# Kernel tuning notes

Hardware: AMD Instinct MI355X
Metric: run time of the kernel (lower is better)

Reference implementation:

```python
import jax, jax.numpy as jnp
import numpy as np
from jax import lax

B, P = 32, 1024          # batch, max_phonemes
V, E, H = 100, 512, 512  # vocab, embedding_dim, hidden_dim
EPS = 1e-5


def setup_inputs() -> dict:
    key = jax.random.key(0)
    ks = jax.random.split(key, 12)
    return {
        "phoneme_ids": jax.random.randint(ks[0], (B, P), 0, V),
        "phoneme_durations": jax.random.randint(ks[1], (B, P), 0, 10),
        "emb": jax.random.normal(ks[2], (V, E), jnp.float32) * 0.02,
        "conv1_w": jax.random.normal(ks[3], (H, E, 3), jnp.float32) * 0.02,
        "conv1_b": jnp.zeros((H,), jnp.float32),
        "bn1_gamma": 1.0 + 0.1 * jax.random.normal(ks[4], (H,), jnp.float32),
        "bn1_beta": 0.1 * jax.random.normal(ks[5], (H,), jnp.float32),
        "bn1_mean": jnp.zeros((H,), jnp.float32),
        "bn1_var": jnp.ones((H,), jnp.float32),
        "conv2_w": jax.random.normal(ks[6], (H, H, 3), jnp.float32) * 0.02,
        "conv2_b": jnp.zeros((H,), jnp.float32),
        "bn2_gamma": 1.0 + 0.1 * jax.random.normal(ks[7], (H,), jnp.float32),
        "bn2_beta": 0.1 * jax.random.normal(ks[8], (H,), jnp.float32),
        "bn2_mean": jnp.zeros((H,), jnp.float32),
        "bn2_var": jnp.ones((H,), jnp.float32),
    }


def _conv_bn_relu(x, w, b, gamma, beta, mean, var):
    # x: [B, C, P]; w: [O, C, 3]; 'same' padding conv1d, inference batchnorm, relu
    y = lax.conv_general_dilated(x, w, (1,), [(1, 1)],
                                 dimension_numbers=("NCH", "OIH", "NCH"))
    y = y + b[None, :, None]
    scale = gamma * lax.rsqrt(var + EPS)
    y = y * scale[None, :, None] + (beta - mean * scale)[None, :, None]
    return jax.nn.relu(y)


def _upsample(x, durations):
    # x: [B, H, P], durations: [B, P] int -> [B, H, max_frames]
    cum = jnp.cumsum(durations, axis=1)              # [B, P]
    total = cum[:, -1]                               # [B]
    max_frames = int(jnp.max(total))                 # concrete (data-derived shape)
    frames = jnp.arange(max_frames)                  # [F]
    # frame f belongs to phoneme p iff cum[p-1] <= f < cum[p]
    idx = jax.vmap(lambda c: jnp.searchsorted(c, frames, side="right"))(cum)
    idx = jnp.minimum(idx, P - 1)                    # [B, F]
    gathered = jnp.take_along_axis(x, idx[:, None, :], axis=2)  # [B, H, F]
    mask = (frames[None, :] < total[:, None]).astype(x.dtype)   # [B, F]
    return gathered * mask[:, None, :]


def reference(phoneme_ids, phoneme_durations, emb,
              conv1_w, conv1_b, bn1_gamma, bn1_beta, bn1_mean, bn1_var,
              conv2_w, conv2_b, bn2_gamma, bn2_beta, bn2_mean, bn2_var):
    x = emb[phoneme_ids]                 # [B, P, E]
    x = jnp.transpose(x, (0, 2, 1))      # [B, E, P]
    x = _conv_bn_relu(x, conv1_w, conv1_b, bn1_gamma, bn1_beta, bn1_mean, bn1_var)
    x = _conv_bn_relu(x, conv2_w, conv2_b, bn2_gamma, bn2_beta, bn2_mean, bn2_var)
    return _upsample(x, phoneme_durations)
```

## Files before the change

kernel.cpp:

```cpp
#include <hip/hip_runtime.h>

#define B_ 32
#define P_ 1024
#define V_ 100
#define E_ 512
#define H_ 512
#define C_ 512
#define EPS_ 1e-5f

typedef float f32x4 __attribute__((ext_vector_type(4)));
typedef short bf16x8 __attribute__((ext_vector_type(8)));

#define GLB(p) ((const __attribute__((address_space(1))) unsigned int*)(p))
#define LDSP(p) ((__attribute__((address_space(3))) unsigned int*)(p))

__device__ __forceinline__ unsigned short f2bf(float f) {
  unsigned int u = __float_as_uint(f);
  u += 0x7fffu + ((u >> 16) & 1u);
  return (unsigned short)(u >> 16);
}
__device__ __forceinline__ float bf2f(unsigned short s) {
  return __uint_as_float(((unsigned int)s) << 16);
}

__global__ __launch_bounds__(256) void w1t_kernel(const float* __restrict__ w1,
                                                  float* __restrict__ w1T) {
  __shared__ float tile[64][65];
  int h0 = blockIdx.x * 64;
  int e0 = blockIdx.y * 64;
  int t = threadIdx.x;
  int c = t & 63, r4 = t >> 6;
#pragma unroll
  for (int r = 0; r < 64; r += 4)
    tile[r + r4][c] = w1[(size_t)(h0 + r + r4) * 1536 + e0 + c];
  __syncthreads();
#pragma unroll
  for (int r = 0; r < 64; r += 4)
    w1T[(size_t)(e0 + r + r4) * 512 + h0 + c] = tile[c][r + r4];
}

__global__ __launch_bounds__(64) void g_kernel(const float* __restrict__ emb,
                                               const float* __restrict__ w1T,
                                               const float* __restrict__ g1,
                                               const float* __restrict__ vr1,
                                               float* __restrict__ G) {
  __shared__ float se[E_];
  int v = blockIdx.x;
  int h = blockIdx.y * 64 + threadIdx.x;
  for (int i = threadIdx.x; i < E_; i += 64) se[i] = emb[(size_t)v * E_ + i];
  __syncthreads();
  float a0 = 0.f, a1 = 0.f, a2 = 0.f;
#pragma unroll 4
  for (int e = 0; e < E_; ++e) {
    float x = se[e];
    const float* wp = w1T + (size_t)(3 * e) * H_ + h;
    a0 = fmaf(wp[0], x, a0);
    a1 = fmaf(wp[H_], x, a1);
    a2 = fmaf(wp[2 * H_], x, a2);
  }
  float sc = g1[h] * rsqrtf(vr1[h] + EPS_);
  G[((size_t)0 * V_ + v) * H_ + h] = a0 * sc;
  G[((size_t)1 * V_ + v) * H_ + h] = a1 * sc;
  G[((size_t)2 * V_ + v) * H_ + h] = a2 * sc;
}

__global__ __launch_bounds__(256) void a2_kernel(
    const float* __restrict__ w2, const float* __restrict__ b1,
    const float* __restrict__ g1, const float* __restrict__ be1,
    const float* __restrict__ mn1, const float* __restrict__ vr1,
    const float* __restrict__ b2, const float* __restrict__ g2,
    const float* __restrict__ be2, const float* __restrict__ mn2,
    const float* __restrict__ vr2, float* __restrict__ bias1,
    float* __restrict__ bias2, unsigned short* __restrict__ A2h,
    unsigned short* __restrict__ A2l) {
  int h = blockIdx.x;
  int tid = threadIdx.x;
  float sc1 = g1[h] * rsqrtf(vr1[h] + EPS_);
  float sc2 = g2[h] * rsqrtf(vr2[h] + EPS_);
  if (tid == 0) {
    bias1[h] = b1[h] * sc1 + be1[h] - mn1[h] * sc1;
    bias2[h] = b2[h] * sc2 + be2[h] - mn2[h] * sc2;
  }
  for (int j = tid; j < 3 * C_; j += 256) {
    int k = j >> 9;
    int c = j & (C_ - 1);
    float val = w2[((size_t)h * C_ + c) * 3 + k] * sc2;
    unsigned short hi = f2bf(val);
    A2h[(size_t)h * (3 * C_) + j] = hi;
    A2l[(size_t)h * (3 * C_) + j] = f2bf(val - bf2f(hi));
  }
}

__global__ __launch_bounds__(256) void embed_conv1_kernel(
    const int* __restrict__ ids, const float* __restrict__ G,
    const float* __restrict__ bias1, unsigned short* __restrict__ Bh,
    unsigned short* __restrict__ Bl) {
  int r = blockIdx.x % (P_ + 2);
  int b = blockIdx.x / (P_ + 2);
  int t = threadIdx.x;
  size_t outbase = ((size_t)b * (P_ + 2) + r) * C_;
  unsigned int* BhU = (unsigned int*)(Bh + outbase);
  unsigned int* BlU = (unsigned int*)(Bl + outbase);
  if (r == 0 || r == P_ + 1) {
    BhU[t] = 0u;
    BlU[t] = 0u;
    return;
  }
  int p = r - 1;
  int v0 = (p >= 1) ? ids[b * P_ + p - 1] : -1;
  int v1 = ids[b * P_ + p];
  int v2 = (p + 1 < P_) ? ids[b * P_ + p + 1] : -1;
  const float2* G0 = (v0 >= 0) ? (const float2*)(G + ((size_t)0 * V_ + v0) * H_) : nullptr;
  const float2* G1 = (const float2*)(G + ((size_t)1 * V_ + v1) * H_);
  const float2* G2 = (v2 >= 0) ? (const float2*)(G + ((size_t)2 * V_ + v2) * H_) : nullptr;
  const float2* bi = (const float2*)bias1;

  float2 s = bi[t];
  float2 gm = G1[t];
  s.x += gm.x;
  s.y += gm.y;
  if (G0) {
    float2 g0 = G0[t];
    s.x += g0.x;
    s.y += g0.y;
  }
  if (G2) {
    float2 g2v = G2[t];
    s.x += g2v.x;
    s.y += g2v.y;
  }
  s.x = fmaxf(s.x, 0.f);
  s.y = fmaxf(s.y, 0.f);
  unsigned short h0 = f2bf(s.x), h1 = f2bf(s.y);
  unsigned short l0 = f2bf(s.x - bf2f(h0)), l1 = f2bf(s.y - bf2f(h1));
  BhU[t] = (unsigned int)h0 | ((unsigned int)h1 << 16);
  BlU[t] = (unsigned int)l0 | ((unsigned int)l1 << 16);
}

__global__ __launch_bounds__(1024) void cumsum_kernel(const int* __restrict__ dur,
                                                      int* __restrict__ cum) {
  __shared__ int s[P_];
  int b = blockIdx.x;
  int t = threadIdx.x;
  s[t] = dur[b * P_ + t];
  __syncthreads();
  for (int off = 1; off < P_; off <<= 1) {
    int v = (t >= off) ? s[t - off] : 0;
    __syncthreads();
    s[t] += v;
    __syncthreads();
  }
  cum[b * P_ + t] = s[t];
}

#define BM 128
#define BN 128
#define BK 32
__global__ __launch_bounds__(256) void conv2_gemm_kernel(
    const unsigned short* __restrict__ A2h, const unsigned short* __restrict__ A2l,
    const unsigned short* __restrict__ Bh, const unsigned short* __restrict__ Bl,
    const float* __restrict__ bias2, float* __restrict__ out2) {
  __shared__ __align__(16) unsigned short lds[4][BM * BK];

  int tid = threadIdx.x;
  int w = tid >> 6;
  int l = tid & 63;

  int bid = blockIdx.x;
  int wg = ((bid & 7) << 7) | (bid >> 3);
  int m0 = (wg >> 8) * BM;
  int n0 = (wg & 255) * BN;
  int b = n0 >> 10;
  int p0 = n0 & (P_ - 1);

  const unsigned short* Ah_base = A2h + (size_t)m0 * (3 * C_);
  const unsigned short* Al_base = A2l + (size_t)m0 * (3 * C_);
  const unsigned short* Bh_base = Bh + ((size_t)b * (P_ + 2) + p0) * C_;
  const unsigned short* Bl_base = Bl + ((size_t)b * (P_ + 2) + p0) * C_;

  f32x4 acc[4][4] = {};

  int srow = l >> 2;
  int scol = (l & 3) * 8;
  int fr = l & 15, fq = l >> 4;
  int wr = (w >> 1) * 64, wc = (w & 1) * 64;

  for (int kt = 0; kt < (3 * C_) / BK; ++kt) {
    int kofs = kt * BK;
#pragma unroll
    for (int q = 0; q < 2; ++q) {
      int seg = q * 4 + w;
      int row = seg * 16 + srow;
      int col = kofs + scol;
      __builtin_amdgcn_global_load_lds(GLB(Ah_base + (size_t)row * (3 * C_) + col),
                                       LDSP(&lds[0][seg * 512]), 16, 0, 0);
      __builtin_amdgcn_global_load_lds(GLB(Al_base + (size_t)row * (3 * C_) + col),
                                       LDSP(&lds[1][seg * 512]), 16, 0, 0);
      __builtin_amdgcn_global_load_lds(GLB(Bh_base + (size_t)row * C_ + col),
                                       LDSP(&lds[2][seg * 512]), 16, 0, 0);
      __builtin_amdgcn_global_load_lds(GLB(Bl_base + (size_t)row * C_ + col),
                                       LDSP(&lds[3][seg * 512]), 16, 0, 0);
    }
    __syncthreads();

    bf16x8 ah[4], al[4], bh[4], bl[4];
#pragma unroll
    for (int i = 0; i < 4; ++i) {
      ah[i] = *(const bf16x8*)&lds[0][(wr + i * 16 + fr) * BK + fq * 8];
      al[i] = *(const bf16x8*)&lds[1][(wr + i * 16 + fr) * BK + fq * 8];
    }
#pragma unroll
    for (int j = 0; j < 4; ++j) {
      bh[j] = *(const bf16x8*)&lds[2][(wc + j * 16 + fr) * BK + fq * 8];
      bl[j] = *(const bf16x8*)&lds[3][(wc + j * 16 + fr) * BK + fq * 8];
    }
#pragma unroll
    for (int i = 0; i < 4; ++i)
#pragma unroll
      for (int j = 0; j < 4; ++j) {
        acc[i][j] = __builtin_amdgcn_mfma_f32_16x16x32_bf16(ah[i], bh[j], acc[i][j], 0, 0, 0);
        acc[i][j] = __builtin_amdgcn_mfma_f32_16x16x32_bf16(ah[i], bl[j], acc[i][j], 0, 0, 0);
        acc[i][j] = __builtin_amdgcn_mfma_f32_16x16x32_bf16(al[i], bh[j], acc[i][j], 0, 0, 0);
      }
    __syncthreads();
  }

#pragma unroll
  for (int i = 0; i < 4; ++i) {
#pragma unroll
    for (int j = 0; j < 4; ++j) {
#pragma unroll
      for (int r = 0; r < 4; ++r) {
        int m = m0 + wr + i * 16 + fq * 4 + r;
        int n = n0 + wc + j * 16 + fr;
        int bb = n >> 10;
        int p = n & (P_ - 1);
        float v = acc[i][j][r] + bias2[m];
        v = fmaxf(v, 0.f);
        out2[((size_t)bb * H_ + m) * P_ + p] = v;
      }
    }
  }
}

__global__ __launch_bounds__(256) void upsample_kernel(const float* __restrict__ out2,
                                                       const int* __restrict__ cum,
                                                       float* __restrict__ out, int T) {
  __shared__ int sc[P_];
  int b = blockIdx.y;
  int tid = threadIdx.x;
  for (int i = tid; i < P_; i += 256) sc[i] = cum[b * P_ + i];
  __syncthreads();
  int t = blockIdx.x * 256 + tid;
  if (t >= T) return;
  int tot = sc[P_ - 1];
  bool valid = (t < tot);
  int idx = 0;
  if (valid) {
    int lo = 0, hi = P_;
    while (lo < hi) {
      int mid = (lo + hi) >> 1;
      if (sc[mid] <= t) lo = mid + 1; else hi = mid;
    }
    idx = min(lo, P_ - 1);
  }
  const float* src = out2 + (size_t)b * H_ * P_ + idx;
  float* dst = out + (size_t)b * H_ * T + t;
  if (valid) {
    for (int h = 0; h < H_; ++h) dst[(size_t)h * T] = src[(size_t)h * P_];
  } else {
    for (int h = 0; h < H_; ++h) dst[(size_t)h * T] = 0.f;
  }
}

static inline size_t align256(size_t x) { return (x + 255) & ~(size_t)255; }

extern "C" void kernel_launch(void* const* d_in, const int* in_sizes, int n_in,
                              void* d_out, int out_size, void* d_ws, size_t ws_size,
                              hipStream_t stream) {
  const int*   ids = (const int*)d_in[0];
  const int*   dur = (const int*)d_in[1];
  const float* emb = (const float*)d_in[2];
  const float* w1  = (const float*)d_in[3];
  const float* b1  = (const float*)d_in[4];
  const float* g1  = (const float*)d_in[5];
  const float* be1 = (const float*)d_in[6];
  const float* mn1 = (const float*)d_in[7];
  const float* vr1 = (const float*)d_in[8];
  const float* w2  = (const float*)d_in[9];
  const float* b2  = (const float*)d_in[10];
  const float* g2  = (const float*)d_in[11];
  const float* be2 = (const float*)d_in[12];
  const float* mn2 = (const float*)d_in[13];
  const float* vr2 = (const float*)d_in[14];
  float* out = (float*)d_out;

  int T = out_size / (B_ * H_);

  char* ws = (char*)d_ws;
  size_t off = 0;
  auto carve = [&](size_t bytes) { void* p = ws + off; off = align256(off + bytes); return p; };
  float* G              = (float*)carve((size_t)3 * V_ * H_ * 4);
  float* w1T            = (float*)carve((size_t)3 * E_ * H_ * 4);
  float* bias1          = (float*)carve(H_ * 4);
  float* bias2          = (float*)carve(H_ * 4);
  unsigned short* A2h   = (unsigned short*)carve((size_t)H_ * 3 * C_ * 2);
  unsigned short* A2l   = (unsigned short*)carve((size_t)H_ * 3 * C_ * 2);
  unsigned short* Bhv   = (unsigned short*)carve((size_t)B_ * (P_ + 2) * C_ * 2);
  unsigned short* Blv   = (unsigned short*)carve((size_t)B_ * (P_ + 2) * C_ * 2);
  float* out2           = (float*)carve((size_t)B_ * H_ * P_ * 4);
  int* cum              = (int*)carve((size_t)B_ * P_ * 4);

  w1t_kernel<<<dim3(H_ / 64, (3 * E_) / 64), 256, 0, stream>>>(w1, w1T);
  a2_kernel<<<H_, 256, 0, stream>>>(w2, b1, g1, be1, mn1, vr1, b2, g2, be2, mn2, vr2,
                                    bias1, bias2, A2h, A2l);
  g_kernel<<<dim3(V_, H_ / 64), 64, 0, stream>>>(emb, w1T, g1, vr1, G);
  embed_conv1_kernel<<<B_ * (P_ + 2), 256, 0, stream>>>(ids, G, bias1, Bhv, Blv);
  cumsum_kernel<<<B_, P_, 0, stream>>>(dur, cum);
  conv2_gemm_kernel<<<(B_ * P_ / BN) * (H_ / BM), 256, 0, stream>>>(A2h, A2l, Bhv, Blv,
                                                                    bias2, out2);
  upsample_kernel<<<dim3((T + 255) / 256, B_), 256, 0, stream>>>(out2, cum, out, T);
}
```

Measured before the change: 698.3 us.

## Rewrite conv2 GEMM as 256x256 double-buffered 8-wave pipeline; vectorize upsample per thread

Replaces the 128x128 single-buffer conv2 GEMM with a 256x256 tile, 512-thread kernel. It double-buffers LDS with swizzled layout, interleaves global-to-LDS staging with MFMA quads, and uses explicit barriers and priority hints. The three split-bf16 products are reformulated as a concatenated K loop over hi/lo segments. The upsample kernel now handles four frames per thread to reduce block count and amortize work. The intent is to overlap memory with MFMA and improve reuse, at the cost of more complex synchronization and higher register pressure.

```diff
diff --git a/kernel.cpp b/kernel.cpp
--- a/kernel.cpp
+++ b/kernel.cpp
@@ -119,16 +119,8 @@
   float2 gm = G1[t];
   s.x += gm.x;
   s.y += gm.y;
-  if (G0) {
-    float2 g0 = G0[t];
-    s.x += g0.x;
-    s.y += g0.y;
-  }
-  if (G2) {
-    float2 g2v = G2[t];
-    s.x += g2v.x;
-    s.y += g2v.y;
-  }
+  if (G0) { float2 g0 = G0[t]; s.x += g0.x; s.y += g0.y; }
+  if (G2) { float2 g2v = G2[t]; s.x += g2v.x; s.y += g2v.y; }
   s.x = fmaxf(s.x, 0.f);
   s.y = fmaxf(s.y, 0.f);
   unsigned short h0 = f2bf(s.x), h1 = f2bf(s.y);
@@ -153,94 +145,182 @@
   cum[b * P_ + t] = s[t];
 }
 
-#define BM 128
-#define BN 128
-#define BK 32
-__global__ __launch_bounds__(256) void conv2_gemm_kernel(
+struct BTrue  { static constexpr bool v = true;  };
+struct BFalse { static constexpr bool v = false; };
+
+__global__ __launch_bounds__(512, 2) void conv2_gemm8_kernel(
     const unsigned short* __restrict__ A2h, const unsigned short* __restrict__ A2l,
     const unsigned short* __restrict__ Bh, const unsigned short* __restrict__ Bl,
     const float* __restrict__ bias2, float* __restrict__ out2) {
-  __shared__ __align__(16) unsigned short lds[4][BM * BK];
-
-  int tid = threadIdx.x;
-  int w = tid >> 6;
-  int l = tid & 63;
+  __shared__ __align__(16) unsigned short sm[4][16384];
+
+  const int tid = threadIdx.x;
+  const int wid = tid >> 6;
+  const int lane = tid & 63;
+  const int wm = wid >> 2, wn = wid & 3;
+  const int fr = lane & 15, fq = lane >> 4;
 
   int bid = blockIdx.x;
-  int wg = ((bid & 7) << 7) | (bid >> 3);
-  int m0 = (wg >> 8) * BM;
-  int n0 = (wg & 255) * BN;
-  int b = n0 >> 10;
+  int wg = (bid & 7) * 32 + (bid >> 3);
+  int m0 = (wg & 1) * 256;
+  int n0 = (wg >> 1) * 256;
+  int bb = n0 >> 10;
   int p0 = n0 & (P_ - 1);
 
-  const unsigned short* Ah_base = A2h + (size_t)m0 * (3 * C_);
-  const unsigned short* Al_base = A2l + (size_t)m0 * (3 * C_);
-  const unsigned short* Bh_base = Bh + ((size_t)b * (P_ + 2) + p0) * C_;
-  const unsigned short* Bl_base = Bl + ((size_t)b * (P_ + 2) + p0) * C_;
-
-  f32x4 acc[4][4] = {};
-
-  int srow = l >> 2;
-  int scol = (l & 3) * 8;
-  int fr = l & 15, fq = l >> 4;
-  int wr = (w >> 1) * 64, wc = (w & 1) * 64;
-
-  for (int kt = 0; kt < (3 * C_) / BK; ++kt) {
-    int kofs = kt * BK;
-#pragma unroll
-    for (int q = 0; q < 2; ++q) {
-      int seg = q * 4 + w;
-      int row = seg * 16 + srow;
-      int col = kofs + scol;
-      __builtin_amdgcn_global_load_lds(GLB(Ah_base + (size_t)row * (3 * C_) + col),
-                                       LDSP(&lds[0][seg * 512]), 16, 0, 0);
-      __builtin_amdgcn_global_load_lds(GLB(Al_base + (size_t)row * (3 * C_) + col),
-                                       LDSP(&lds[1][seg * 512]), 16, 0, 0);
-      __builtin_amdgcn_global_load_lds(GLB(Bh_base + (size_t)row * C_ + col),
-                                       LDSP(&lds[2][seg * 512]), 16, 0, 0);
-      __builtin_amdgcn_global_load_lds(GLB(Bl_base + (size_t)row * C_ + col),
-                                       LDSP(&lds[3][seg * 512]), 16, 0, 0);
+  const unsigned short* Arow_h = A2h + (size_t)m0 * 1536;
+  const unsigned short* Arow_l = A2l + (size_t)m0 * 1536;
+  const size_t boff = ((size_t)bb * (P_ + 2) + p0) * 512;
+  const unsigned short* Brow_h = Bh + boff;
+  const unsigned short* Brow_l = Bl + boff;
+
+  const int srow = tid >> 3;
+  const int scol = (((tid & 7) ^ ((tid >> 3) & 7))) * 8;
+  const int ldsw = wid * 512;
+
+  auto stageA = [&](int kt, int blk) {
+    const unsigned short* base = (kt < 48) ? Arow_h : Arow_l;
+    int kl = (kt % 24) * 64;
+    const unsigned short* src = base + (size_t)(blk * 64 + srow) * 1536 + kl + scol;
+    __builtin_amdgcn_global_load_lds(GLB(src), LDSP(&sm[kt & 1][blk * 4096 + ldsw]), 16, 0, 0);
+  };
+  auto stageB = [&](int kt, int blk) {
+    const unsigned short* base = (kt >= 24 && kt < 48) ? Brow_l : Brow_h;
+    int kl = (kt % 24) * 64;
+    const unsigned short* src = base + (size_t)(blk * 64 + srow) * 512 + kl + scol;
+    __builtin_amdgcn_global_load_lds(GLB(src), LDSP(&sm[2 + (kt & 1)][blk * 4096 + ldsw]), 16, 0, 0);
+  };
+
+  f32x4 acc[8][4] = {};
+
+  const int rA0 = wm * 128 + fr;
+  const int rB0 = wn * 64 + fr;
+  const int cxor = fr & 7;
+
+  auto rdA = [&](bf16x8 (&af)[4][2], int buf, int mh) {
+#pragma unroll
+    for (int m = 0; m < 4; ++m)
+#pragma unroll
+      for (int ks = 0; ks < 2; ++ks)
+        af[m][ks] = *(const bf16x8*)&sm[buf][(rA0 + mh * 64 + m * 16) * 64 +
+                                            ((ks * 4 + fq) ^ cxor) * 8];
+  };
+  auto rdB = [&](bf16x8 (&bv)[2][2], int buf, int nh) {
+#pragma unroll
+    for (int n = 0; n < 2; ++n)
+#pragma unroll
+      for (int ks = 0; ks < 2; ++ks)
+        bv[n][ks] = *(const bf16x8*)&sm[2 + buf][(rB0 + nh * 32 + n * 16) * 64 +
+                                                 ((ks * 4 + fq) ^ cxor) * 8];
+  };
+
+#define SYNC_HEAD()                                      \
+  __builtin_amdgcn_sched_barrier(0);                     \
+  __builtin_amdgcn_s_barrier();                          \
+  asm volatile("s_waitcnt lgkmcnt(0)" ::: "memory");     \
+  __builtin_amdgcn_sched_barrier(0);                     \
+  __builtin_amdgcn_s_setprio(1)
+
+#define SYNC_TAIL()                                      \
+  __builtin_amdgcn_s_setprio(0);                         \
+  __builtin_amdgcn_sched_barrier(0);                     \
+  __builtin_amdgcn_s_barrier();                          \
+  __builtin_amdgcn_sched_barrier(0)
+
+#define MFMA_QUAD(mh, nh, AF, BF)                                              \
+  _Pragma("unroll") for (int m = 0; m < 4; ++m)                                \
+  _Pragma("unroll") for (int n = 0; n < 2; ++n)                                \
+  _Pragma("unroll") for (int ks = 0; ks < 2; ++ks)                             \
+    acc[(mh) * 4 + m][(nh) * 2 + n] = __builtin_amdgcn_mfma_f32_16x16x32_bf16( \
+        AF[m][ks], BF[n][ks], acc[(mh) * 4 + m][(nh) * 2 + n], 0, 0, 0)
+
+#pragma unroll
+  for (int blk = 0; blk < 4; ++blk) { stageA(0, blk); stageB(0, blk); }
+  stageA(1, 0); stageA(1, 2);
+  asm volatile("s_waitcnt vmcnt(2)" ::: "memory");
+  __builtin_amdgcn_sched_barrier(0);
+  __builtin_amdgcn_s_barrier();
+  __builtin_amdgcn_sched_barrier(0);
+
+  int kt = 0;
+  auto iter = [&](auto lasttag) {
+    constexpr bool LAST = decltype(lasttag)::v;
+    bf16x8 af[4][2], bv[2][2];
+    rdA(af, 0, 0); rdB(bv, 0, 0);
+    stageA(kt + 1, 1); stageA(kt + 1, 3); stageB(kt + 1, 0);
+    SYNC_HEAD(); MFMA_QUAD(0, 0, af, bv); SYNC_TAIL();
+
+    rdB(bv, 0, 1);
+    stageB(kt + 1, 1); stageB(kt + 1, 2); stageB(kt + 1, 3);
+    SYNC_HEAD(); MFMA_QUAD(0, 1, af, bv); SYNC_TAIL();
+
+    rdA(af, 0, 1); rdB(bv, 0, 0);
+    if constexpr (!LAST) { stageA(kt + 2, 0); stageA(kt + 2, 2); }
+    SYNC_HEAD(); MFMA_QUAD(1, 0, af, bv); SYNC_TAIL();
+
+    rdB(bv, 0, 1);
+    __builtin_amdgcn_sched_barrier(0);
+    __builtin_amdgcn_s_barrier();
+    asm volatile("s_waitcnt lgkmcnt(0)" ::: "memory");
+    __builtin_amdgcn_sched_barrier(0);
+    __builtin_amdgcn_s_setprio(1);
+    MFMA_QUAD(1, 1, af, bv);
+    __builtin_amdgcn_s_setprio(0);
+    __builtin_amdgcn_sched_barrier(0);
+    if constexpr (LAST) asm volatile("s_waitcnt vmcnt(0)" ::: "memory");
+    else                asm volatile("s_waitcnt vmcnt(2)" ::: "memory");
+    __builtin_amdgcn_s_barrier();
+    __builtin_amdgcn_sched_barrier(0);
+
+    rdA(af, 1, 0); rdB(bv, 1, 0);
+    if constexpr (!LAST) { stageA(kt + 2, 1); stageA(kt + 2, 3); stageB(kt + 2, 0); }
+    SYNC_HEAD(); MFMA_QUAD(0, 0, af, bv); SYNC_TAIL();
+
+    rdB(bv, 1, 1);
+    if constexpr (!LAST) { stageB(kt + 2, 1); stageB(kt + 2, 2); stageB(kt + 2, 3); }
+    SYNC_HEAD(); MFMA_QUAD(0, 1, af, bv); SYNC_TAIL();
+
+    rdA(af, 1, 1); rdB(bv, 1, 0);
+    if constexpr (!LAST) { stageA(kt + 3, 0); stageA(kt + 3, 2); }
+    SYNC_HEAD(); MFMA_QUAD(1, 0, af, bv); SYNC_TAIL();
+
+    rdB(bv, 1, 1);
+    __builtin_amdgcn_sched_barrier(0);
+    __builtin_amdgcn_s_barrier();
+    asm volatile("s_waitcnt lgkmcnt(0)" ::: "memory");
+    __builtin_amdgcn_sched_barrier(0);
+    __builtin_amdgcn_s_setprio(1);
+    MFMA_QUAD(1, 1, af, bv);
+    __builtin_amdgcn_s_setprio(0);
+    __builtin_amdgcn_sched_barrier(0);
+    if constexpr (!LAST) {
+      asm volatile("s_waitcnt vmcnt(2)" ::: "memory");
+      __builtin_amdgcn_s_barrier();
+      __builtin_amdgcn_sched_barrier(0);
     }
-    __syncthreads();
-
-    bf16x8 ah[4], al[4], bh[4], bl[4];
-#pragma unroll
-    for (int i = 0; i < 4; ++i) {
-      ah[i] = *(const bf16x8*)&lds[0][(wr + i * 16 + fr) * BK + fq * 8];
-      al[i] = *(const bf16x8*)&lds[1][(wr + i * 16 + fr) * BK + fq * 8];
-    }
-#pragma unroll
-    for (int j = 0; j < 4; ++j) {
-      bh[j] = *(const bf16x8*)&lds[2][(wc + j * 16 + fr) * BK + fq * 8];
-      bl[j] = *(const bf16x8*)&lds[3][(wc + j * 16 + fr) * BK + fq * 8];
-    }
-#pragma unroll
-    for (int i = 0; i < 4; ++i)
-#pragma unroll
-      for (int j = 0; j < 4; ++j) {
-        acc[i][j] = __builtin_amdgcn_mfma_f32_16x16x32_bf16(ah[i], bh[j], acc[i][j], 0, 0, 0);
-        acc[i][j] = __builtin_amdgcn_mfma_f32_16x16x32_bf16(ah[i], bl[j], acc[i][j], 0, 0, 0);
-        acc[i][j] = __builtin_amdgcn_mfma_f32_16x16x32_bf16(al[i], bh[j], acc[i][j], 0, 0, 0);
-      }
-    __syncthreads();
-  }
-
-#pragma unroll
-  for (int i = 0; i < 4; ++i) {
-#pragma unroll
-    for (int j = 0; j < 4; ++j) {
+    kt += 2;
+  };
+
+  for (int i = 0; i < 35; ++i) iter(BFalse{});
+  iter(BTrue{});
+
+#pragma unroll
+  for (int ai = 0; ai < 8; ++ai) {
+    int row = m0 + wm * 128 + (ai >> 2) * 64 + (ai & 3) * 16 + fq * 4;
+#pragma unroll
+    for (int bj = 0; bj < 4; ++bj) {
+      int col = n0 + wn * 64 + (bj >> 1) * 32 + (bj & 1) * 16 + fr;
+      int bb2 = col >> 10;
+      int p = col & (P_ - 1);
 #pragma unroll
       for (int r = 0; r < 4; ++r) {
-        int m = m0 + wr + i * 16 + fq * 4 + r;
-        int n = n0 + wc + j * 16 + fr;
-        int bb = n >> 10;
-        int p = n & (P_ - 1);
-        float v = acc[i][j][r] + bias2[m];
-        v = fmaxf(v, 0.f);
-        out2[((size_t)bb * H_ + m) * P_ + p] = v;
+        float v = acc[ai][bj][r] + bias2[row + r];
+        out2[((size_t)bb2 * H_ + row + r) * P_ + p] = fmaxf(v, 0.f);
       }
     }
   }
+#undef SYNC_HEAD
+#undef SYNC_TAIL
+#undef MFMA_QUAD
 }
 
 __global__ __launch_bounds__(256) void upsample_kernel(const float* __restrict__ out2,
@@ -251,25 +331,41 @@
   int tid = threadIdx.x;
   for (int i = tid; i < P_; i += 256) sc[i] = cum[b * P_ + i];
   __syncthreads();
-  int t = blockIdx.x * 256 + tid;
-  if (t >= T) return;
+  int t0 = (blockIdx.x * 256 + tid) * 4;
+  if (t0 >= T) return;
   int tot = sc[P_ - 1];
-  bool valid = (t < tot);
-  int idx = 0;
-  if (valid) {
+  int idx[4];
+  bool val[4];
+#pragma unroll
+  for (int u = 0; u < 4; ++u) {
+    int t = t0 + u;
+    val[u] = (t < T) && (t < tot);
     int lo = 0, hi = P_;
     while (lo < hi) {
       int mid = (lo + hi) >> 1;
       if (sc[mid] <= t) lo = mid + 1; else hi = mid;
     }
-    idx = min(lo, P_ - 1);
-  }
-  const float* src = out2 + (size_t)b * H_ * P_ + idx;
-  float* dst = out + (size_t)b * H_ * T + t;
-  if (valid) {
-    for (int h = 0; h < H_; ++h) dst[(size_t)h * T] = src[(size_t)h * P_];
+    idx[u] = min(lo, P_ - 1);
+  }
+  const float* src = out2 + (size_t)b * H_ * P_;
+  float* dst = out + (size_t)b * H_ * T + t0;
+  if (t0 + 3 < T) {
+#pragma unroll 2
+    for (int h = 0; h < H_; ++h) {
+      const float* sr = src + (size_t)h * P_;
+      float* dr = dst + (size_t)h * T;
+      dr[0] = val[0] ? sr[idx[0]] : 0.f;
+      dr[1] = val[1] ? sr[idx[1]] : 0.f;
+      dr[2] = val[2] ? sr[idx[2]] : 0.f;
+      dr[3] = val[3] ? sr[idx[3]] : 0.f;
+    }
   } else {
-    for (int h = 0; h < H_; ++h) dst[(size_t)h * T] = 0.f;
+    int nrem = T - t0;
+    for (int h = 0; h < H_; ++h) {
+      const float* sr = src + (size_t)h * P_;
+      float* dr = dst + (size_t)h * T;
+      for (int u = 0; u < nrem; ++u) dr[u] = val[u] ? sr[idx[u]] : 0.f;
+    }
   }
 }
 
@@ -317,7 +413,6 @@
   g_kernel<<<dim3(V_, H_ / 64), 64, 0, stream>>>(emb, w1T, g1, vr1, G);
   embed_conv1_kernel<<<B_ * (P_ + 2), 256, 0, stream>>>(ids, G, bias1, Bhv, Blv);
   cumsum_kernel<<<B_, P_, 0, stream>>>(dur, cum);
-  conv2_gemm_kernel<<<(B_ * P_ / BN) * (H_ / BM), 256, 0, stream>>>(A2h, A2l, Bhv, Blv,
-                                                                    bias2, out2);
-  upsample_kernel<<<dim3((T + 255) / 256, B_), 256, 0, stream>>>(out2, cum, out, T);
-}
+  conv2_gemm8_kernel<<<256, 512, 0, stream>>>(A2h, A2l, Bhv, Blv, bias2, out2);
+  upsample_kernel<<<dim3((T + 1023) / 1024, B_), 256, 0, stream>>>(out2, cum, out, T);
+}
```

Result: slower. 1.163 ms (+66.6%).
